# Performance work log

Hardware: AMD Instinct MI355X
Metric: run time of the kernel (lower is better)

## Reference

```python
import jax, jax.numpy as jnp
import numpy as np
from jax import lax

H = 128


def _ema_scan(x):
    # x: [B, T, N, F] -> EMA along T: s_t = 0.9*s_{t-1} + 0.1*x_t
    xt = jnp.moveaxis(x, 1, 0)  # [T, B, N, F]

    def step(s, xi):
        s = s * 0.9 + xi * 0.1
        return s, s

    _, ys = lax.scan(step, jnp.zeros_like(xt[0]), xt)
    return jnp.moveaxis(ys, 0, 1)  # [B, T, N, F]


def setup_inputs() -> dict:
    key = jax.random.key(0)
    k1, k2, k3, k4, k5 = jax.random.split(key, 5)
    B, T, N = 4, 96, 512
    x = jax.random.normal(k1, (B, T, N, H), dtype=jnp.float32)
    s = 1.0 / np.sqrt(H)
    W_exp = jax.random.uniform(k2, (2 * H, H), jnp.float32, -s, s)
    b_exp = jax.random.uniform(k3, (2 * H,), jnp.float32, -s, s)
    W_con = jax.random.uniform(k4, (H, H), jnp.float32, -s, s)
    b_con = jax.random.uniform(k5, (H,), jnp.float32, -s, s)
    return {"spatial_temporal_representation": x, "W_exp": W_exp, "b_exp": b_exp,
            "W_con": W_con, "b_con": b_con}


def reference(spatial_temporal_representation, W_exp, b_exp, W_con, b_con):
    x = spatial_temporal_representation  # [B,T,N,H]
    expanded = jnp.einsum('btnh,oh->btno', x, W_exp) + b_exp  # [B,T,N,2H]
    state_primary, state_gating = jnp.split(expanded, 2, axis=-1)
    gated_activation = jax.nn.sigmoid(_ema_scan(state_gating))
    out = jnp.einsum('btnh,oh->btno', state_primary * gated_activation, W_con) + b_con
    return out
```

## Files before the change

### kernel.cpp

```cpp
#include <hip/hip_runtime.h>

#define B_DIM 4
#define T_DIM 96
#define N_DIM 512
#define H_DIM 128
#define LDS_STRIDE 136

typedef __attribute__((ext_vector_type(8))) short short8;
typedef __attribute__((ext_vector_type(4))) float f32x4;

__device__ __forceinline__ unsigned short f2b(float f) {
    union { float f; unsigned u; } c; c.f = f;
    unsigned u = c.u;
    unsigned r = (u + 0x7FFFu + ((u >> 16) & 1u)) >> 16;
    return (unsigned short)r;
}
__device__ __forceinline__ float b2f(unsigned short s) {
    union { unsigned u; float f; } c; c.u = ((unsigned)s) << 16;
    return c.f;
}

extern "C" __global__ __launch_bounds__(256, 2)
void mamba_fused(const float* __restrict__ x,
                 const float* __restrict__ W_exp,
                 const float* __restrict__ b_exp,
                 const float* __restrict__ W_con,
                 const float* __restrict__ b_con,
                 float* __restrict__ out)
{
    __shared__ unsigned short xs[T_DIM * LDS_STRIDE];
    __shared__ unsigned short prim[T_DIM * LDS_STRIDE];
    __shared__ unsigned short gate[T_DIM * LDS_STRIDE];

    const int tid  = threadIdx.x;
    const int wave = tid >> 6;
    const int lane = tid & 63;
    const int q    = lane >> 4;
    const int l16  = lane & 15;

    const int blk = blockIdx.x;
    const int n   = blk & (N_DIM - 1);
    const int b   = blk >> 9;

    const float* xg = x + ((size_t)b * T_DIM * N_DIM + (size_t)n) * H_DIM;

    for (int idx = tid; idx < T_DIM * (H_DIM / 4); idx += 256) {
        int t  = idx >> 5;
        int c4 = (idx & 31) << 2;
        float4 v = *(const float4*)(xg + (size_t)t * (N_DIM * H_DIM) + c4);
        ushort4 u;
        u.x = f2b(v.x); u.y = f2b(v.y); u.z = f2b(v.z); u.w = f2b(v.w);
        *(ushort4*)&xs[t * LDS_STRIDE + c4] = u;
    }

    short8 wf[4][4];
    float  bias1[4][4];
    {
        const int obase = wave * 64;
        for (int ot = 0; ot < 4; ++ot) {
            const float* wrow = W_exp + (size_t)(obase + ot * 16 + l16) * H_DIM + q * 8;
            for (int k0 = 0; k0 < 4; ++k0) {
                float4 v0 = *(const float4*)(wrow + k0 * 32);
                float4 v1 = *(const float4*)(wrow + k0 * 32 + 4);
                short8 f;
                f[0] = (short)f2b(v0.x); f[1] = (short)f2b(v0.y);
                f[2] = (short)f2b(v0.z); f[3] = (short)f2b(v0.w);
                f[4] = (short)f2b(v1.x); f[5] = (short)f2b(v1.y);
                f[6] = (short)f2b(v1.z); f[7] = (short)f2b(v1.w);
                wf[ot][k0] = f;
            }
            for (int r = 0; r < 4; ++r)
                bias1[ot][r] = b_exp[obase + ot * 16 + q * 4 + r];
        }
    }
    __syncthreads();

    for (int mt = 0; mt < 6; ++mt) {
        short8 bfr[4];
        const unsigned short* arow = &xs[(mt * 16 + l16) * LDS_STRIDE];
        for (int k0 = 0; k0 < 4; ++k0)
            bfr[k0] = *(const short8*)(arow + k0 * 32 + q * 8);
        const int tcol = mt * 16 + l16;
        for (int ot = 0; ot < 4; ++ot) {
            f32x4 acc = {0.f, 0.f, 0.f, 0.f};
            for (int k0 = 0; k0 < 4; ++k0)
                acc = __builtin_amdgcn_mfma_f32_16x16x32_bf16(wf[ot][k0], bfr[k0], acc, 0, 0, 0);
            const int o = wave * 64 + ot * 16 + q * 4;
            ushort4 pk;
            pk.x = f2b(acc[0] + bias1[ot][0]);
            pk.y = f2b(acc[1] + bias1[ot][1]);
            pk.z = f2b(acc[2] + bias1[ot][2]);
            pk.w = f2b(acc[3] + bias1[ot][3]);
            unsigned short* dst = (o < H_DIM) ? prim : gate;
            *(ushort4*)&dst[tcol * LDS_STRIDE + (o & (H_DIM - 1))] = pk;
        }
    }
    __syncthreads();

    short8 wc[2][4];
    float  bias2[2][4];
    {
        const int obase = wave * 32;
        for (int ot = 0; ot < 2; ++ot) {
            const float* wrow = W_con + (size_t)(obase + ot * 16 + l16) * H_DIM + q * 8;
            for (int k0 = 0; k0 < 4; ++k0) {
                float4 v0 = *(const float4*)(wrow + k0 * 32);
                float4 v1 = *(const float4*)(wrow + k0 * 32 + 4);
                short8 f;
                f[0] = (short)f2b(v0.x); f[1] = (short)f2b(v0.y);
                f[2] = (short)f2b(v0.z); f[3] = (short)f2b(v0.w);
                f[4] = (short)f2b(v1.x); f[5] = (short)f2b(v1.y);
                f[6] = (short)f2b(v1.z); f[7] = (short)f2b(v1.w);
                wc[ot][k0] = f;
            }
            for (int r = 0; r < 4; ++r)
                bias2[ot][r] = b_con[obase + ot * 16 + q * 4 + r];
        }
    }

    if (tid < H_DIM) {
        const int h = tid;
        float s = 0.f;
        #pragma unroll 4
        for (int t = 0; t < T_DIM; ++t) {
            float g = b2f(gate[t * LDS_STRIDE + h]);
            s = 0.9f * s + 0.1f * g;
            float sig = 1.f / (1.f + __expf(-s));
            float p = b2f(prim[t * LDS_STRIDE + h]);
            xs[t * LDS_STRIDE + h] = f2b(p * sig);
        }
    }
    __syncthreads();

    float* og = out + ((size_t)b * T_DIM * N_DIM + (size_t)n) * H_DIM;
    for (int mt = 0; mt < 6; ++mt) {
        short8 bfr[4];
        const unsigned short* arow = &xs[(mt * 16 + l16) * LDS_STRIDE];
        for (int k0 = 0; k0 < 4; ++k0)
            bfr[k0] = *(const short8*)(arow + k0 * 32 + q * 8);
        const int t = mt * 16 + l16;
        for (int ot = 0; ot < 2; ++ot) {
            f32x4 acc = {0.f, 0.f, 0.f, 0.f};
            for (int k0 = 0; k0 < 4; ++k0)
                acc = __builtin_amdgcn_mfma_f32_16x16x32_bf16(wc[ot][k0], bfr[k0], acc, 0, 0, 0);
            const int o = wave * 32 + ot * 16 + q * 4;
            float4 v;
            v.x = acc[0] + bias2[ot][0];
            v.y = acc[1] + bias2[ot][1];
            v.z = acc[2] + bias2[ot][2];
            v.w = acc[3] + bias2[ot][3];
            *(float4*)(og + (size_t)t * (N_DIM * H_DIM) + o) = v;
        }
    }
}

extern "C" void kernel_launch(void* const* d_in, const int* in_sizes, int n_in,
                              void* d_out, int out_size, void* d_ws, size_t ws_size,
                              hipStream_t stream) {
    const float* x     = (const float*)d_in[0];
    const float* W_exp = (const float*)d_in[1];
    const float* b_exp = (const float*)d_in[2];
    const float* W_con = (const float*)d_in[3];
    const float* b_con = (const float*)d_in[4];
    float* out = (float*)d_out;

    dim3 grid(B_DIM * N_DIM);
    dim3 block(256);
    hipLaunchKernelGGL(mamba_fused, grid, block, 0, stream,
                       x, W_exp, b_exp, W_con, b_con, out);
}
```

Baseline: 252.6 us.

## Replace serial EMA scan with decay-matrix MFMA and pre-convert weights to bf16

```diff
diff --git a/kernel.cpp b/kernel.cpp
--- a/kernel.cpp
+++ b/kernel.cpp
@@ -4,33 +4,56 @@
 #define T_DIM 96
 #define N_DIM 512
 #define H_DIM 128
-#define LDS_STRIDE 136
+#define NH    (N_DIM * H_DIM)
+
+#define WS_WEXP  0
+#define WS_WCON  32768
+#define WS_L     49152
+#define WS_TOTAL 58368
 
 typedef __attribute__((ext_vector_type(8))) short short8;
 typedef __attribute__((ext_vector_type(4))) float f32x4;
 
-__device__ __forceinline__ unsigned short f2b(float f) {
+__device__ __forceinline__ unsigned short f2b_rh(float f) {
     union { float f; unsigned u; } c; c.f = f;
-    unsigned u = c.u;
-    unsigned r = (u + 0x7FFFu + ((u >> 16) & 1u)) >> 16;
-    return (unsigned short)r;
+    return (unsigned short)((c.u + 0x8000u) >> 16);
+}
+__device__ __forceinline__ unsigned pack_bf16_2(float a, float b) {
+    union { float f; unsigned u; } ca, cb; ca.f = a; cb.f = b;
+    return __builtin_amdgcn_perm(cb.u + 0x8000u, ca.u + 0x8000u, 0x07060302u);
 }
 __device__ __forceinline__ float b2f(unsigned short s) {
     union { unsigned u; float f; } c; c.u = ((unsigned)s) << 16;
     return c.f;
 }
 
-extern "C" __global__ __launch_bounds__(256, 2)
+extern "C" __global__ void prep_kernel(const float* __restrict__ Wexp,
+                                       const float* __restrict__ Wcon,
+                                       unsigned short* __restrict__ ws) {
+    int i = blockIdx.x * 256 + threadIdx.x;
+    if (i < 32768) {
+        ws[WS_WEXP + i] = f2b_rh(Wexp[i]);
+    } else if (i < 49152) {
+        int j = i - 32768;
+        ws[WS_WCON + j] = f2b_rh(Wcon[j]);
+    } else if (i < WS_TOTAL) {
+        int j = i - 49152;
+        int t = j / 96, k = j - t * 96;
+        float v = 0.0f;
+        if (k <= t) v = 0.1f * __expf((float)(t - k) * -0.1053605157f);
+        ws[WS_L + j] = f2b_rh(v);
+    }
+}
+
+extern "C" __global__ __launch_bounds__(256, 3)
 void mamba_fused(const float* __restrict__ x,
-                 const float* __restrict__ W_exp,
+                 const unsigned short* __restrict__ ws,
                  const float* __restrict__ b_exp,
-                 const float* __restrict__ W_con,
                  const float* __restrict__ b_con,
                  float* __restrict__ out)
 {
-    __shared__ unsigned short xs[T_DIM * LDS_STRIDE];
-    __shared__ unsigned short prim[T_DIM * LDS_STRIDE];
-    __shared__ unsigned short gate[T_DIM * LDS_STRIDE];
+    __shared__ __align__(16) unsigned short prim[T_DIM * 136];
+    __shared__ __align__(16) unsigned short gpg[H_DIM * 104];
 
     const int tid  = threadIdx.x;
     const int wave = tid >> 6;
@@ -44,90 +67,106 @@
 
     const float* xg = x + ((size_t)b * T_DIM * N_DIM + (size_t)n) * H_DIM;
 
-    for (int idx = tid; idx < T_DIM * (H_DIM / 4); idx += 256) {
-        int t  = idx >> 5;
-        int c4 = (idx & 31) << 2;
-        float4 v = *(const float4*)(xg + (size_t)t * (N_DIM * H_DIM) + c4);
-        ushort4 u;
-        u.x = f2b(v.x); u.y = f2b(v.y); u.z = f2b(v.z); u.w = f2b(v.w);
-        *(ushort4*)&xs[t * LDS_STRIDE + c4] = u;
-    }
-
     short8 wf[4][4];
-    float  bias1[4][4];
+    float4 bias1[4];
     {
         const int obase = wave * 64;
+        const unsigned short* wsW = ws + WS_WEXP;
         for (int ot = 0; ot < 4; ++ot) {
-            const float* wrow = W_exp + (size_t)(obase + ot * 16 + l16) * H_DIM + q * 8;
-            for (int k0 = 0; k0 < 4; ++k0) {
-                float4 v0 = *(const float4*)(wrow + k0 * 32);
-                float4 v1 = *(const float4*)(wrow + k0 * 32 + 4);
-                short8 f;
-                f[0] = (short)f2b(v0.x); f[1] = (short)f2b(v0.y);
-                f[2] = (short)f2b(v0.z); f[3] = (short)f2b(v0.w);
-                f[4] = (short)f2b(v1.x); f[5] = (short)f2b(v1.y);
-                f[6] = (short)f2b(v1.z); f[7] = (short)f2b(v1.w);
-                wf[ot][k0] = f;
-            }
-            for (int r = 0; r < 4; ++r)
-                bias1[ot][r] = b_exp[obase + ot * 16 + q * 4 + r];
-        }
-    }
-    __syncthreads();
+            const unsigned short* wrow = wsW + (size_t)(obase + ot * 16 + l16) * H_DIM + q * 8;
+            for (int k0 = 0; k0 < 4; ++k0)
+                wf[ot][k0] = *(const short8*)(wrow + k0 * 32);
+            bias1[ot] = *(const float4*)(b_exp + obase + ot * 16 + q * 4);
+        }
+    }
 
     for (int mt = 0; mt < 6; ++mt) {
+        const float* xrow = xg + (size_t)(mt * 16 + l16) * NH + q * 8;
         short8 bfr[4];
-        const unsigned short* arow = &xs[(mt * 16 + l16) * LDS_STRIDE];
-        for (int k0 = 0; k0 < 4; ++k0)
-            bfr[k0] = *(const short8*)(arow + k0 * 32 + q * 8);
+        for (int k0 = 0; k0 < 4; ++k0) {
+            float4 v0 = *(const float4*)(xrow + k0 * 32);
+            float4 v1 = *(const float4*)(xrow + k0 * 32 + 4);
+            union { unsigned u[4]; short8 s; } p;
+            p.u[0] = pack_bf16_2(v0.x, v0.y);
+            p.u[1] = pack_bf16_2(v0.z, v0.w);
+            p.u[2] = pack_bf16_2(v1.x, v1.y);
+            p.u[3] = pack_bf16_2(v1.z, v1.w);
+            bfr[k0] = p.s;
+        }
         const int tcol = mt * 16 + l16;
         for (int ot = 0; ot < 4; ++ot) {
             f32x4 acc = {0.f, 0.f, 0.f, 0.f};
             for (int k0 = 0; k0 < 4; ++k0)
                 acc = __builtin_amdgcn_mfma_f32_16x16x32_bf16(wf[ot][k0], bfr[k0], acc, 0, 0, 0);
             const int o = wave * 64 + ot * 16 + q * 4;
-            ushort4 pk;
-            pk.x = f2b(acc[0] + bias1[ot][0]);
-            pk.y = f2b(acc[1] + bias1[ot][1]);
-            pk.z = f2b(acc[2] + bias1[ot][2]);
-            pk.w = f2b(acc[3] + bias1[ot][3]);
-            unsigned short* dst = (o < H_DIM) ? prim : gate;
-            *(ushort4*)&dst[tcol * LDS_STRIDE + (o & (H_DIM - 1))] = pk;
+            float r0 = acc[0] + bias1[ot].x, r1 = acc[1] + bias1[ot].y;
+            float r2 = acc[2] + bias1[ot].z, r3 = acc[3] + bias1[ot].w;
+            if (wave < 2) {
+                union { unsigned u[2]; ushort4 s; } pk;
+                pk.u[0] = pack_bf16_2(r0, r1);
+                pk.u[1] = pack_bf16_2(r2, r3);
+                *(ushort4*)&prim[tcol * 136 + o] = pk.s;
+            } else {
+                const int g = o - 128;
+                gpg[(g + 0) * 104 + tcol] = f2b_rh(r0);
+                gpg[(g + 1) * 104 + tcol] = f2b_rh(r1);
+                gpg[(g + 2) * 104 + tcol] = f2b_rh(r2);
+                gpg[(g + 3) * 104 + tcol] = f2b_rh(r3);
+            }
         }
     }
     __syncthreads();
 
+    f32x4 eacc[2][6];
+    for (int ht = 0; ht < 2; ++ht)
+        for (int tt = 0; tt < 6; ++tt)
+            eacc[ht][tt] = (f32x4){0.f, 0.f, 0.f, 0.f};
+    {
+        const unsigned short* wsL = ws + WS_L;
+        for (int kf = 0; kf < 3; ++kf) {
+            short8 af[2];
+            for (int ht = 0; ht < 2; ++ht) {
+                const int h = (wave * 2 + ht) * 16 + l16;
+                af[ht] = *(const short8*)&gpg[h * 104 + kf * 32 + q * 8];
+            }
+            for (int tt = 0; tt < 6; ++tt) {
+                short8 bf = *(const short8*)(wsL + (size_t)(tt * 16 + l16) * 96 + kf * 32 + q * 8);
+                eacc[0][tt] = __builtin_amdgcn_mfma_f32_16x16x32_bf16(af[0], bf, eacc[0][tt], 0, 0, 0);
+                eacc[1][tt] = __builtin_amdgcn_mfma_f32_16x16x32_bf16(af[1], bf, eacc[1][tt], 0, 0, 0);
+            }
+        }
+    }
+
     short8 wc[2][4];
-    float  bias2[2][4];
+    float4 bias2[2];
     {
         const int obase = wave * 32;
+        const unsigned short* wsW = ws + WS_WCON;
         for (int ot = 0; ot < 2; ++ot) {
-            const float* wrow = W_con + (size_t)(obase + ot * 16 + l16) * H_DIM + q * 8;
-            for (int k0 = 0; k0 < 4; ++k0) {
-                float4 v0 = *(const float4*)(wrow + k0 * 32);
-                float4 v1 = *(const float4*)(wrow + k0 * 32 + 4);
-                short8 f;
-                f[0] = (short)f2b(v0.x); f[1] = (short)f2b(v0.y);
-                f[2] = (short)f2b(v0.z); f[3] = (short)f2b(v0.w);
-                f[4] = (short)f2b(v1.x); f[5] = (short)f2b(v1.y);
-                f[6] = (short)f2b(v1.z); f[7] = (short)f2b(v1.w);
-                wc[ot][k0] = f;
-            }
-            for (int r = 0; r < 4; ++r)
-                bias2[ot][r] = b_con[obase + ot * 16 + q * 4 + r];
-        }
-    }
-
-    if (tid < H_DIM) {
-        const int h = tid;
-        float s = 0.f;
-        #pragma unroll 4
-        for (int t = 0; t < T_DIM; ++t) {
-            float g = b2f(gate[t * LDS_STRIDE + h]);
-            s = 0.9f * s + 0.1f * g;
-            float sig = 1.f / (1.f + __expf(-s));
-            float p = b2f(prim[t * LDS_STRIDE + h]);
-            xs[t * LDS_STRIDE + h] = f2b(p * sig);
+            const unsigned short* wrow = wsW + (size_t)(obase + ot * 16 + l16) * H_DIM + q * 8;
+            for (int k0 = 0; k0 < 4; ++k0)
+                wc[ot][k0] = *(const short8*)(wrow + k0 * 32);
+            bias2[ot] = *(const float4*)(b_con + obase + ot * 16 + q * 4);
+        }
+    }
+    __syncthreads();
+
+    for (int ht = 0; ht < 2; ++ht) {
+        const int hb = (wave * 2 + ht) * 16 + q * 4;
+        for (int tt = 0; tt < 6; ++tt) {
+            const int t = tt * 16 + l16;
+            ushort4 pv = *(const ushort4*)&prim[t * 136 + hb];
+            f32x4 s = eacc[ht][tt];
+            float sg0 = __fdividef(1.f, 1.f + __expf(-s[0]));
+            float sg1 = __fdividef(1.f, 1.f + __expf(-s[1]));
+            float sg2 = __fdividef(1.f, 1.f + __expf(-s[2]));
+            float sg3 = __fdividef(1.f, 1.f + __expf(-s[3]));
+            float p0 = b2f(pv.x) * sg0, p1 = b2f(pv.y) * sg1;
+            float p2 = b2f(pv.z) * sg2, p3 = b2f(pv.w) * sg3;
+            union { unsigned u[2]; ushort4 s; } pk;
+            pk.u[0] = pack_bf16_2(p0, p1);
+            pk.u[1] = pack_bf16_2(p2, p3);
+            *(ushort4*)&gpg[t * 136 + hb] = pk.s;
         }
     }
     __syncthreads();
@@ -135,9 +174,9 @@
     float* og = out + ((size_t)b * T_DIM * N_DIM + (size_t)n) * H_DIM;
     for (int mt = 0; mt < 6; ++mt) {
         short8 bfr[4];
-        const unsigned short* arow = &xs[(mt * 16 + l16) * LDS_STRIDE];
+        const unsigned short* prow = &gpg[(mt * 16 + l16) * 136];
         for (int k0 = 0; k0 < 4; ++k0)
-            bfr[k0] = *(const short8*)(arow + k0 * 32 + q * 8);
+            bfr[k0] = *(const short8*)(prow + k0 * 32 + q * 8);
         const int t = mt * 16 + l16;
         for (int ot = 0; ot < 2; ++ot) {
             f32x4 acc = {0.f, 0.f, 0.f, 0.f};
@@ -145,11 +184,11 @@
                 acc = __builtin_amdgcn_mfma_f32_16x16x32_bf16(wc[ot][k0], bfr[k0], acc, 0, 0, 0);
             const int o = wave * 32 + ot * 16 + q * 4;
             float4 v;
-            v.x = acc[0] + bias2[ot][0];
-            v.y = acc[1] + bias2[ot][1];
-            v.z = acc[2] + bias2[ot][2];
-            v.w = acc[3] + bias2[ot][3];
-            *(float4*)(og + (size_t)t * (N_DIM * H_DIM) + o) = v;
+            v.x = acc[0] + bias2[ot].x;
+            v.y = acc[1] + bias2[ot].y;
+            v.z = acc[2] + bias2[ot].z;
+            v.w = acc[3] + bias2[ot].w;
+            *(float4*)(og + (size_t)t * NH + o) = v;
         }
     }
 }
@@ -163,9 +202,10 @@
     const float* W_con = (const float*)d_in[3];
     const float* b_con = (const float*)d_in[4];
     float* out = (float*)d_out;
-
-    dim3 grid(B_DIM * N_DIM);
-    dim3 block(256);
-    hipLaunchKernelGGL(mamba_fused, grid, block, 0, stream,
-                       x, W_exp, b_exp, W_con, b_con, out);
-}
+    unsigned short* ws = (unsigned short*)d_ws;
+
+    hipLaunchKernelGGL(prep_kernel, dim3(WS_TOTAL / 256), dim3(256), 0, stream,
+                       W_exp, W_con, ws);
+    hipLaunchKernelGGL(mamba_fused, dim3(B_DIM * N_DIM), dim3(256), 0, stream,
+                       x, ws, b_exp, b_con, out);
+}
```

After: 230.5 us. -8.7%, faster.
